# Kernel optimization log

Hardware: AMD Instinct MI355X
Metric: run time of the kernel (lower is better)

## Reference

```python
import jax, jax.numpy as jnp
import numpy as np

NEG = -1e9  # mask value for non-edges (matches masked_fill(-inf) numerically-safely)
SLOPE = 0.2  # LeakyReLU negative slope in GraphAttentionLayer


def gat_layer(x, W, a_l, a_r, adj, n_heads):
    """One GraphAttentionLayer (eval mode, is_concat=True).
    e[i,j,h] = leakyrelu(a_l . g[i,h] + a_r . g[j,h])  (attn Linear split into halves)
    softmax over j masked by adj, then aggregate neighbors.
    """
    n = x.shape[0]
    g = (x @ W).reshape(n, n_heads, -1)          # [n, h, f]
    el = jnp.einsum('ihf,f->ih', g, a_l)          # score contribution of node i
    er = jnp.einsum('jhf,f->jh', g, a_r)          # score contribution of node j
    e = jax.nn.leaky_relu(el[:, None, :] + er[None, :, :], SLOPE)  # [n, n, h]
    e = jnp.where(adj[:, :, None] != 0, e, NEG)
    a = jax.nn.softmax(e, axis=1)                 # softmax over neighbors j
    out = jnp.einsum('ijh,jhf->ihf', a, g)        # weighted aggregation
    return out.reshape(n, -1)                     # concat heads


def setup_inputs() -> dict:
    key = jax.random.key(0)
    ks = jax.random.split(key, 8)
    N, IN, HID, OUT, H = 2048, 512, 256, 128, 8
    x = jax.random.normal(ks[0], (N, IN), dtype=jnp.float32)
    adj = jax.random.randint(ks[1], (N, N), 0, 2, dtype=jnp.int32)
    adj = adj.at[jnp.arange(N), jnp.arange(N)].set(1)  # self loops: no empty softmax rows
    s = 0.05
    W1 = jax.random.normal(ks[2], (IN, HID), dtype=jnp.float32) * s
    a1_l = jax.random.normal(ks[3], (HID // H,), dtype=jnp.float32) * s
    a1_r = jax.random.normal(ks[4], (HID // H,), dtype=jnp.float32) * s
    W2 = jax.random.normal(ks[5], (HID, OUT), dtype=jnp.float32) * s
    a2_l = jax.random.normal(ks[6], (OUT,), dtype=jnp.float32) * s
    a2_r = jax.random.normal(ks[7], (OUT,), dtype=jnp.float32) * s
    return {"x": x, "W1": W1, "a1_l": a1_l, "a1_r": a1_r,
            "W2": W2, "a2_l": a2_l, "a2_r": a2_r, "adj_mat": adj}


def reference(x, W1, a1_l, a1_r, W2, a2_l, a2_r, adj_mat):
    # eval mode: nn.Dropout is identity
    h = gat_layer(x, W1, a1_l, a1_r, adj_mat, n_heads=8)
    h = jax.nn.elu(h)
    out = gat_layer(h, W2, a2_l, a2_r, adj_mat, n_heads=1)
    return out
```

## Files before the change

### kernel.cpp

```cpp
#include <hip/hip_runtime.h>
#include <hip/hip_bf16.h>

#define NN 2048
typedef unsigned short u16;
typedef unsigned long long u64;
typedef __attribute__((ext_vector_type(8))) short short8;
typedef __attribute__((ext_vector_type(4))) float f32x4;

__device__ __forceinline__ unsigned bfb(float x) {
    unsigned u = __float_as_uint(x);
    return (u + 0x7FFFu + ((u >> 16) & 1u)) >> 16;
}

__global__ __launch_bounds__(256) void prep(const float* __restrict__ x,
                                            const float* __restrict__ W1,
                                            const float* __restrict__ W2,
                                            const int* __restrict__ adj,
                                            u16* __restrict__ xb, u16* __restrict__ w1t,
                                            u16* __restrict__ w2t, u64* __restrict__ ab) {
    const int b = blockIdx.x;
    if (b < 16384) {
        int t = b * 256 + threadIdx.x;
        int W = t >> 6, lane = t & 63;
        int i = W >> 5, jw = W & 31;
        int a = adj[(size_t)i * NN + jw * 64 + lane];
        u64 m = __ballot(a != 0);
        if (lane == 0) ab[(size_t)i * 32 + jw] = m;
    } else if (b < 16384 + 1024) {
        int t = (b - 16384) * 256 + threadIdx.x;
        float4 v = ((const float4*)x)[t];
        uint2 o;
        o.x = bfb(v.x) | (bfb(v.y) << 16);
        o.y = bfb(v.z) | (bfb(v.w) << 16);
        ((uint2*)xb)[t] = o;
    } else if (b < 16384 + 1024 + 512) {
        int u = (b - 17408) * 256 + threadIdx.x;
        int c = u >> 9, k = u & 511;
        w1t[u] = (u16)bfb(W1[(size_t)k * 256 + c]);
    } else {
        int u = (b - 17920) * 256 + threadIdx.x;
        int c = u >> 8, k = u & 255;
        w2t[u] = (u16)bfb(W2[(size_t)k * 128 + c]);
    }
}

__global__ __launch_bounds__(256) void gemm1(const u16* __restrict__ A,
                                             const u16* __restrict__ BT,
                                             const float* __restrict__ al,
                                             const float* __restrict__ ar,
                                             u16* __restrict__ GT,
                                             float* __restrict__ el,
                                             float* __restrict__ ert) {
    const int i0 = blockIdx.x * 16, cs = blockIdx.y;
    const int t = threadIdx.x, lane = t & 63, w = t >> 6;
    const int q = lane >> 4, n = lane & 15;
    const int ct = w & 1, kh = w >> 1;
    __shared__ float osh[2][16][16];
    __shared__ float pel[2][16], per_[2][16];

    const u16* ap = A + (size_t)(i0 + n) * 512 + kh * 256 + q * 8;
    const u16* bp = BT + (size_t)(cs * 32 + ct * 16 + n) * 512 + kh * 256 + q * 8;
    f32x4 acc = {0.f, 0.f, 0.f, 0.f};
#pragma unroll
    for (int ks = 0; ks < 8; ++ks) {
        short8 a = *(const short8*)(ap + ks * 32);
        short8 b = *(const short8*)(bp + ks * 32);
        acc = __builtin_amdgcn_mfma_f32_16x16x32_bf16(a, b, acc, 0, 0, 0);
    }
    if (kh == 1) {
#pragma unroll
        for (int r = 0; r < 4; ++r) osh[ct][q * 4 + r][n] = acc[r];
    }
    __syncthreads();
    if (kh == 0) {
#pragma unroll
        for (int r = 0; r < 4; ++r) acc[r] += osh[ct][q * 4 + r][n];
        uint2 g0;
        g0.x = bfb(acc[0]) | (bfb(acc[1]) << 16);
        g0.y = bfb(acc[2]) | (bfb(acc[3]) << 16);
        *(uint2*)&GT[(size_t)(cs * 32 + ct * 16 + n) * NN + i0 + q * 4] = g0;
        const float alv = al[ct * 16 + n], arv = ar[ct * 16 + n];
#pragma unroll
        for (int r = 0; r < 4; ++r) {
            float ve = acc[r] * alv, vr = acc[r] * arv;
#pragma unroll
            for (int off = 1; off <= 8; off <<= 1) {
                ve += __shfl_xor(ve, off);
                vr += __shfl_xor(vr, off);
            }
            if (n == 0) { pel[ct][q * 4 + r] = ve; per_[ct][q * 4 + r] = vr; }
        }
    }
    __syncthreads();
    if (t < 16) {
        el[(size_t)(i0 + t) * 8 + cs] = pel[0][t] + pel[1][t];
        ert[(size_t)cs * NN + i0 + t] = per_[0][t] + per_[1][t];
    }
}

__global__ __launch_bounds__(256) void gemm2(const u16* __restrict__ A,
                                             const u16* __restrict__ BT,
                                             const float* __restrict__ al,
                                             const float* __restrict__ ar,
                                             u16* __restrict__ GT,
                                             float* __restrict__ el,
                                             float* __restrict__ ert) {
    const int i0 = blockIdx.x * 16, cs = blockIdx.y;
    const int t = threadIdx.x, lane = t & 63, w = t >> 6;
    const int q = lane >> 4, n = lane & 15;
    const int ct = w & 1, kh = w >> 1;
    __shared__ float osh[2][16][16];
    __shared__ float pel[2][16], per_[2][16];

    const u16* ap = A + (size_t)(i0 + n) * 256 + kh * 128 + q * 8;
    const u16* bp = BT + (size_t)(cs * 32 + ct * 16 + n) * 256 + kh * 128 + q * 8;
    f32x4 acc = {0.f, 0.f, 0.f, 0.f};
#pragma unroll
    for (int ks = 0; ks < 4; ++ks) {
        short8 a = *(const short8*)(ap + ks * 32);
        short8 b = *(const short8*)(bp + ks * 32);
        acc = __builtin_amdgcn_mfma_f32_16x16x32_bf16(a, b, acc, 0, 0, 0);
    }
    if (kh == 1) {
#pragma unroll
        for (int r = 0; r < 4; ++r) osh[ct][q * 4 + r][n] = acc[r];
    }
    __syncthreads();
    if (kh == 0) {
#pragma unroll
        for (int r = 0; r < 4; ++r) acc[r] += osh[ct][q * 4 + r][n];
        uint2 g0;
        g0.x = bfb(acc[0]) | (bfb(acc[1]) << 16);
        g0.y = bfb(acc[2]) | (bfb(acc[3]) << 16);
        *(uint2*)&GT[(size_t)(cs * 32 + ct * 16 + n) * NN + i0 + q * 4] = g0;
        const float alv = al[cs * 32 + ct * 16 + n], arv = ar[cs * 32 + ct * 16 + n];
#pragma unroll
        for (int r = 0; r < 4; ++r) {
            float ve = acc[r] * alv, vr = acc[r] * arv;
#pragma unroll
            for (int off = 1; off <= 8; off <<= 1) {
                ve += __shfl_xor(ve, off);
                vr += __shfl_xor(vr, off);
            }
            if (n == 0) { pel[ct][q * 4 + r] = ve; per_[ct][q * 4 + r] = vr; }
        }
    }
    __syncthreads();
    if (t < 16) {
        atomicAdd(&el[i0 + t], pel[0][t] + pel[1][t]);
        atomicAdd(&ert[i0 + t], per_[0][t] + per_[1][t]);
    }
}

__global__ __launch_bounds__(512) void attn1(const float* __restrict__ el,
                                             const float* __restrict__ ert,
                                             const unsigned* __restrict__ ab32,
                                             const u16* __restrict__ gbt,
                                             u16* __restrict__ hbb) {
    const int rt = blockIdx.x, sec = blockIdx.y;
    const int i0 = rt * 16, h0 = sec * 2;
    const int t = threadIdx.x, lane = t & 63, w = t >> 6;
    const int q = lane >> 4, n = lane & 15;
    const int m = t >> 5, jq = t & 31;
    const int hl = w >> 2, ch = (w >> 1) & 1, kf = w & 1;

    __shared__ __align__(16) float ers[2 * 2048];
    __shared__ __align__(16) u16 pl[2][16][72];
    __shared__ unsigned absh[16][64];
    __shared__ float psum_sh[16][2];
    __shared__ float osh[2][2][16][16];
    __shared__ float wmax[2][8];
    __shared__ float mxsh[2];

    float4 v0 = *(const float4*)(ert + (size_t)h0 * NN + t * 4);
    float4 v1 = *(const float4*)(ert + (size_t)(h0 + 1) * NN + t * 4);
    *(float4*)&ers[t * 4] = v0;
    *(float4*)&ers[2048 + t * 4] = v1;
    float m0 = fmaxf(fmaxf(v0.x, v0.y), fmaxf(v0.z, v0.w));
    float m1 = fmaxf(fmaxf(v1.x, v1.y), fmaxf(v1.z, v1.w));
#pragma unroll
    for (int off = 32; off; off >>= 1) {
        m0 = fmaxf(m0, __shfl_xor(m0, off));
        m1 = fmaxf(m1, __shfl_xor(m1, off));
    }
    if (lane == 0) { wmax[0][w] = m0; wmax[1][w] = m1; }
    for (int c = t; c < 1024; c += 512)
        absh[c >> 6][c & 63] = ab32[(size_t)(i0 + (c >> 6)) * 64 + (c & 63)];
    __syncthreads();
    if (t < 2) {
        float mm = wmax[t][0];
#pragma unroll
        for (int ww = 1; ww < 8; ++ww) mm = fmaxf(mm, wmax[t][ww]);
        mxsh[t] = mm;
    }
    __syncthreads();

    float elv[2], mxv[2], ps[2];
#pragma unroll
    for (int h = 0; h < 2; ++h) {
        float e = el[(size_t)(i0 + m) * 8 + h0 + h];
        elv[h] = e;
        float mm = e + mxsh[h];
        mxv[h] = fmaxf(mm, 0.2f * mm);
        ps[h] = 0.f;
    }
    const int col = sec * 64 + hl * 32 + ch * 16 + n;
    const u16* gb = gbt + (size_t)col * NN + kf * 32 + q * 8;
    short8 bc = *(const short8*)gb;
    f32x4 acc = {0.f, 0.f, 0.f, 0.f};

    for (int tile = 0; tile < 32; ++tile) {
        const int jt = tile * 64;
        short8 bn = bc;
        if (tile < 31) bn = *(const short8*)(gb + jt + 64);
        unsigned word = absh[m][tile * 2 + (jq >> 4)];
        unsigned bits = (word >> ((2 * jq) & 31)) & 3u;
#pragma unroll
        for (int h = 0; h < 2; ++h) {
            float2 e2 = *(const float2*)&ers[h * 2048 + jt + 2 * jq];
            float s0 = elv[h] + e2.x, s1 = elv[h] + e2.y;
            s0 = fmaxf(s0, 0.2f * s0) - mxv[h];
            s1 = fmaxf(s1, 0.2f * s1) - mxv[h];
            float p0 = (bits & 1u) ? __expf(s0) : 0.f;
            float p1 = (bits & 2u) ? __expf(s1) : 0.f;
            ps[h] += p0 + p1;
            *(unsigned*)&pl[h][m][2 * jq] = bfb(p0) | (bfb(p1) << 16);
        }
        __syncthreads();
        short8 a = *(const short8*)&pl[hl][n][kf * 32 + q * 8];
        acc = __builtin_amdgcn_mfma_f32_16x16x32_bf16(a, bc, acc, 0, 0, 0);
        bc = bn;
        __syncthreads();
    }

#pragma unroll
    for (int h = 0; h < 2; ++h) {
        float v = ps[h];
#pragma unroll
        for (int off = 16; off; off >>= 1) v += __shfl_down(v, off, 32);
        if (jq == 0) psum_sh[m][h] = v;
    }
    if (kf == 1) {
#pragma unroll
        for (int r = 0; r < 4; ++r) osh[hl][ch][q * 4 + r][n] = acc[r];
    }
    __syncthreads();
    if (kf == 0) {
#pragma unroll
        for (int r = 0; r < 4; ++r) {
            int mr = q * 4 + r;
            float o = (acc[r] + osh[hl][ch][mr][n]) / psum_sh[mr][hl];
            o = o > 0.f ? o : (__expf(o) - 1.f);
            hbb[(size_t)(i0 + mr) * 256 + col] = (u16)bfb(o);
        }
    }
}

__global__ __launch_bounds__(512) void attn2(const float* __restrict__ el,
                                             const float* __restrict__ ert,
                                             const unsigned* __restrict__ ab32,
                                             const u16* __restrict__ gbt,
                                             float* __restrict__ out) {
    const int rt = blockIdx.x, sec = blockIdx.y;
    const int i0 = rt * 16;
    const int t = threadIdx.x, lane = t & 63, w = t >> 6;
    const int q = lane >> 4, n = lane & 15;
    const int m = t >> 5, jq = t & 31;
    const int ct = w >> 2, kfr = w & 3;

    __shared__ __align__(16) float ers[2048];
    __shared__ __align__(16) u16 pl[16][136];
    __shared__ unsigned absh[16][64];
    __shared__ float psum_sh[16];
    __shared__ float osh[2][3][16][16];
    __shared__ float wmax[8];
    __shared__ float mxsh;

    float4 v0 = *(const float4*)(ert + t * 4);
    *(float4*)&ers[t * 4] = v0;
    float m0 = fmaxf(fmaxf(v0.x, v0.y), fmaxf(v0.z, v0.w));
#pragma unroll
    for (int off = 32; off; off >>= 1) m0 = fmaxf(m0, __shfl_xor(m0, off));
    if (lane == 0) wmax[w] = m0;
    for (int c = t; c < 1024; c += 512)
        absh[c >> 6][c & 63] = ab32[(size_t)(i0 + (c >> 6)) * 64 + (c & 63)];
    __syncthreads();
    if (t == 0) {
        float mm = wmax[0];
#pragma unroll
        for (int ww = 1; ww < 8; ++ww) mm = fmaxf(mm, wmax[ww]);
        mxsh = mm;
    }
    __syncthreads();

    const float elv = el[i0 + m];
    float mm2 = elv + mxsh;
    const float mxv = fmaxf(mm2, 0.2f * mm2);
    float ps = 0.f;
    const int col = sec * 32 + ct * 16 + n;
    const u16* gb = gbt + (size_t)col * NN + kfr * 32 + q * 8;
    short8 bc = *(const short8*)gb;
    f32x4 acc = {0.f, 0.f, 0.f, 0.f};

    for (int tile = 0; tile < 16; ++tile) {
        const int jt = tile * 128;
        short8 bn = bc;
        if (tile < 15) bn = *(const short8*)(gb + jt + 128);
        unsigned word = absh[m][tile * 4 + (jq >> 3)];
        unsigned bits = (word >> ((jq & 7) * 4)) & 0xFu;
        float4 e4 = *(const float4*)&ers[jt + jq * 4];
        float s0 = elv + e4.x, s1 = elv + e4.y, s2 = elv + e4.z, s3 = elv + e4.w;
        s0 = fmaxf(s0, 0.2f * s0) - mxv;
        s1 = fmaxf(s1, 0.2f * s1) - mxv;
        s2 = fmaxf(s2, 0.2f * s2) - mxv;
        s3 = fmaxf(s3, 0.2f * s3) - mxv;
        float p0 = (bits & 1u) ? __expf(s0) : 0.f;
        float p1 = (bits & 2u) ? __expf(s1) : 0.f;
        float p2 = (bits & 4u) ? __expf(s2) : 0.f;
        float p3 = (bits & 8u) ? __expf(s3) : 0.f;
        ps += (p0 + p1) + (p2 + p3);
        uint2 pk;
        pk.x = bfb(p0) | (bfb(p1) << 16);
        pk.y = bfb(p2) | (bfb(p3) << 16);
        *(uint2*)&pl[m][jq * 4] = pk;
        __syncthreads();
        short8 a = *(const short8*)&pl[n][kfr * 32 + q * 8];
        acc = __builtin_amdgcn_mfma_f32_16x16x32_bf16(a, bc, acc, 0, 0, 0);
        bc = bn;
        __syncthreads();
    }

#pragma unroll
    for (int off = 16; off; off >>= 1) ps += __shfl_down(ps, off, 32);
    if (jq == 0) psum_sh[m] = ps;
    if (kfr > 0) {
#pragma unroll
        for (int r = 0; r < 4; ++r) osh[ct][kfr - 1][q * 4 + r][n] = acc[r];
    }
    __syncthreads();
    if (kfr == 0) {
#pragma unroll
        for (int r = 0; r < 4; ++r) {
            int mr = q * 4 + r;
            float o = acc[r] + osh[ct][0][mr][n] + osh[ct][1][mr][n] + osh[ct][2][mr][n];
            out[(size_t)(i0 + mr) * 128 + col] = o / psum_sh[mr];
        }
    }
}

extern "C" void kernel_launch(void* const* d_in, const int* in_sizes, int n_in,
                              void* d_out, int out_size, void* d_ws, size_t ws_size,
                              hipStream_t stream) {
    const float* x   = (const float*)d_in[0];
    const float* W1  = (const float*)d_in[1];
    const float* a1l = (const float*)d_in[2];
    const float* a1r = (const float*)d_in[3];
    const float* W2  = (const float*)d_in[4];
    const float* a2l = (const float*)d_in[5];
    const float* a2r = (const float*)d_in[6];
    const int* adj = (const int*)d_in[7];

    char* p = (char*)d_ws;
    u16* xb    = (u16*)p;            p += (size_t)NN * 512 * 2;
    u16* w1t   = (u16*)p;            p += (size_t)256 * 512 * 2;
    u16* w2t   = (u16*)p;            p += (size_t)128 * 256 * 2;
    unsigned* abits = (unsigned*)p;  p += (size_t)NN * 64 * 4;
    u16* gbt1  = (u16*)p;            p += (size_t)256 * NN * 2;
    u16* hbb   = (u16*)p;            p += (size_t)NN * 256 * 2;
    u16* gbt2  = (u16*)p;            p += (size_t)128 * NN * 2;
    float* el1 = (float*)p;          p += (size_t)NN * 8 * 4;
    float* ert1 = (float*)p;         p += (size_t)8 * NN * 4;
    float* el2 = (float*)p;          p += (size_t)NN * 4;
    float* ert2 = (float*)p;         p += (size_t)NN * 4;

    hipMemsetAsync(el2, 0, 2 * NN * sizeof(float), stream);
    prep<<<18048, 256, 0, stream>>>(x, W1, W2, adj, xb, w1t, w2t, (u64*)abits);

    gemm1<<<dim3(128, 8), 256, 0, stream>>>(xb, w1t, a1l, a1r, gbt1, el1, ert1);
    attn1<<<dim3(128, 4), 512, 0, stream>>>(el1, ert1, abits, gbt1, hbb);

    gemm2<<<dim3(128, 4), 256, 0, stream>>>(hbb, w2t, a2l, a2r, gbt2, el2, ert2);
    attn2<<<dim3(128, 4), 512, 0, stream>>>(el2, ert2, abits, gbt2, (float*)d_out);
}
```

Measured before the change: 133.1 us.

## Double-buffer attention probability tiles and widen K tiles in GAT attention kernels

Both attention kernels now double-buffer the shared-memory probability tile, so the next tile's scores are computed while the current tile's MFMAs run, leaving one barrier per tile instead of two. attn1 moves from 64-wide to 128-wide neighbor tiles, with two MFMAs per wave per tile. attn2 is regridded to 2 column sections of 64 columns with a 2-way K split, which halves the redundant softmax work across blocks. The right-side scores are cached in LDS as bf16 rather than fp32, cutting LDS footprint at the cost of a small loss of precision in the attention logits.

```diff
diff --git a/kernel.cpp b/kernel.cpp
--- a/kernel.cpp
+++ b/kernel.cpp
@@ -11,6 +11,7 @@
     unsigned u = __float_as_uint(x);
     return (u + 0x7FFFu + ((u >> 16) & 1u)) >> 16;
 }
+__device__ __forceinline__ unsigned pk2(float a, float b) { return bfb(a) | (bfb(b) << 16); }
 
 __global__ __launch_bounds__(256) void prep(const float* __restrict__ x,
                                             const float* __restrict__ W1,
@@ -30,8 +31,8 @@
         int t = (b - 16384) * 256 + threadIdx.x;
         float4 v = ((const float4*)x)[t];
         uint2 o;
-        o.x = bfb(v.x) | (bfb(v.y) << 16);
-        o.y = bfb(v.z) | (bfb(v.w) << 16);
+        o.x = pk2(v.x, v.y);
+        o.y = pk2(v.z, v.w);
         ((uint2*)xb)[t] = o;
     } else if (b < 16384 + 1024 + 512) {
         int u = (b - 17408) * 256 + threadIdx.x;
@@ -76,8 +77,8 @@
 #pragma unroll
         for (int r = 0; r < 4; ++r) acc[r] += osh[ct][q * 4 + r][n];
         uint2 g0;
-        g0.x = bfb(acc[0]) | (bfb(acc[1]) << 16);
-        g0.y = bfb(acc[2]) | (bfb(acc[3]) << 16);
+        g0.x = pk2(acc[0], acc[1]);
+        g0.y = pk2(acc[2], acc[3]);
         *(uint2*)&GT[(size_t)(cs * 32 + ct * 16 + n) * NN + i0 + q * 4] = g0;
         const float alv = al[ct * 16 + n], arv = ar[ct * 16 + n];
 #pragma unroll
@@ -130,8 +131,8 @@
 #pragma unroll
         for (int r = 0; r < 4; ++r) acc[r] += osh[ct][q * 4 + r][n];
         uint2 g0;
-        g0.x = bfb(acc[0]) | (bfb(acc[1]) << 16);
-        g0.y = bfb(acc[2]) | (bfb(acc[3]) << 16);
+        g0.x = pk2(acc[0], acc[1]);
+        g0.y = pk2(acc[2], acc[3]);
         *(uint2*)&GT[(size_t)(cs * 32 + ct * 16 + n) * NN + i0 + q * 4] = g0;
         const float alv = al[cs * 32 + ct * 16 + n], arv = ar[cs * 32 + ct * 16 + n];
 #pragma unroll
@@ -162,10 +163,10 @@
     const int t = threadIdx.x, lane = t & 63, w = t >> 6;
     const int q = lane >> 4, n = lane & 15;
     const int m = t >> 5, jq = t & 31;
-    const int hl = w >> 2, ch = (w >> 1) & 1, kf = w & 1;
-
-    __shared__ __align__(16) float ers[2 * 2048];
-    __shared__ __align__(16) u16 pl[2][16][72];
+    const int hl = w >> 2, ch = (w >> 1) & 1, kf2 = w & 1;
+
+    __shared__ u16 ersb[2][2048];
+    __shared__ __align__(16) u16 pl[2][2][16][136];
     __shared__ unsigned absh[16][64];
     __shared__ float psum_sh[16][2];
     __shared__ float osh[2][2][16][16];
@@ -174,8 +175,11 @@
 
     float4 v0 = *(const float4*)(ert + (size_t)h0 * NN + t * 4);
     float4 v1 = *(const float4*)(ert + (size_t)(h0 + 1) * NN + t * 4);
-    *(float4*)&ers[t * 4] = v0;
-    *(float4*)&ers[2048 + t * 4] = v1;
+    uint2 c0, c1;
+    c0.x = pk2(v0.x, v0.y); c0.y = pk2(v0.z, v0.w);
+    c1.x = pk2(v1.x, v1.y); c1.y = pk2(v1.z, v1.w);
+    *(uint2*)&ersb[0][t * 4] = c0;
+    *(uint2*)&ersb[1][t * 4] = c1;
     float m0 = fmaxf(fmaxf(v0.x, v0.y), fmaxf(v0.z, v0.w));
     float m1 = fmaxf(fmaxf(v1.x, v1.y), fmaxf(v1.z, v1.w));
 #pragma unroll
@@ -204,32 +208,59 @@
         mxv[h] = fmaxf(mm, 0.2f * mm);
         ps[h] = 0.f;
     }
-    const int col = sec * 64 + hl * 32 + ch * 16 + n;
-    const u16* gb = gbt + (size_t)col * NN + kf * 32 + q * 8;
-    short8 bc = *(const short8*)gb;
-    f32x4 acc = {0.f, 0.f, 0.f, 0.f};
-
-    for (int tile = 0; tile < 32; ++tile) {
-        const int jt = tile * 64;
-        short8 bn = bc;
-        if (tile < 31) bn = *(const short8*)(gb + jt + 64);
-        unsigned word = absh[m][tile * 2 + (jq >> 4)];
-        unsigned bits = (word >> ((2 * jq) & 31)) & 3u;
+
+    auto stage = [&](int tl, int nb) {
+        unsigned word = absh[m][tl * 4 + (jq >> 3)];
+        unsigned bits = (word >> ((jq & 7) * 4)) & 0xFu;
+        const int jo = tl * 128 + jq * 4;
+        uint2 raw0 = *(const uint2*)&ersb[0][jo];
+        uint2 raw1 = *(const uint2*)&ersb[1][jo];
 #pragma unroll
         for (int h = 0; h < 2; ++h) {
-            float2 e2 = *(const float2*)&ers[h * 2048 + jt + 2 * jq];
-            float s0 = elv[h] + e2.x, s1 = elv[h] + e2.y;
+            uint2 raw = h ? raw1 : raw0;
+            float e0 = __uint_as_float(raw.x << 16);
+            float e1 = __uint_as_float(raw.x & 0xFFFF0000u);
+            float e2 = __uint_as_float(raw.y << 16);
+            float e3 = __uint_as_float(raw.y & 0xFFFF0000u);
+            float s0 = elv[h] + e0, s1 = elv[h] + e1, s2 = elv[h] + e2, s3 = elv[h] + e3;
             s0 = fmaxf(s0, 0.2f * s0) - mxv[h];
             s1 = fmaxf(s1, 0.2f * s1) - mxv[h];
+            s2 = fmaxf(s2, 0.2f * s2) - mxv[h];
+            s3 = fmaxf(s3, 0.2f * s3) - mxv[h];
             float p0 = (bits & 1u) ? __expf(s0) : 0.f;
             float p1 = (bits & 2u) ? __expf(s1) : 0.f;
-            ps[h] += p0 + p1;
-            *(unsigned*)&pl[h][m][2 * jq] = bfb(p0) | (bfb(p1) << 16);
-        }
-        __syncthreads();
-        short8 a = *(const short8*)&pl[hl][n][kf * 32 + q * 8];
-        acc = __builtin_amdgcn_mfma_f32_16x16x32_bf16(a, bc, acc, 0, 0, 0);
-        bc = bn;
+            float p2 = (bits & 4u) ? __expf(s2) : 0.f;
+            float p3 = (bits & 8u) ? __expf(s3) : 0.f;
+            ps[h] += (p0 + p1) + (p2 + p3);
+            uint2 pkv;
+            pkv.x = pk2(p0, p1);
+            pkv.y = pk2(p2, p3);
+            *(uint2*)&pl[nb][h][m][jq * 4] = pkv;
+        }
+    };
+
+    const int col = sec * 64 + hl * 32 + ch * 16 + n;
+    const u16* gb = gbt + (size_t)col * NN + kf2 * 64 + q * 8;
+    short8 bc0 = *(const short8*)gb;
+    short8 bc1 = *(const short8*)(gb + 32);
+    f32x4 acc = {0.f, 0.f, 0.f, 0.f};
+
+    stage(0, 0);
+    __syncthreads();
+
+    for (int tile = 0; tile < 16; ++tile) {
+        short8 bn0 = bc0, bn1 = bc1;
+        if (tile < 15) {
+            bn0 = *(const short8*)(gb + tile * 128 + 128);
+            bn1 = *(const short8*)(gb + tile * 128 + 160);
+        }
+        const u16* ap = &pl[tile & 1][hl][n][kf2 * 64 + q * 8];
+        short8 a0 = *(const short8*)ap;
+        short8 a1 = *(const short8*)(ap + 32);
+        acc = __builtin_amdgcn_mfma_f32_16x16x32_bf16(a0, bc0, acc, 0, 0, 0);
+        acc = __builtin_amdgcn_mfma_f32_16x16x32_bf16(a1, bc1, acc, 0, 0, 0);
+        if (tile < 15) stage(tile + 1, (tile + 1) & 1);
+        bc0 = bn0; bc1 = bn1;
         __syncthreads();
     }
 
@@ -240,12 +271,12 @@
         for (int off = 16; off; off >>= 1) v += __shfl_down(v, off, 32);
         if (jq == 0) psum_sh[m][h] = v;
     }
-    if (kf == 1) {
+    if (kf2 == 1) {
 #pragma unroll
         for (int r = 0; r < 4; ++r) osh[hl][ch][q * 4 + r][n] = acc[r];
     }
     __syncthreads();
-    if (kf == 0) {
+    if (kf2 == 0) {
 #pragma unroll
         for (int r = 0; r < 4; ++r) {
             int mr = q * 4 + r;
@@ -266,18 +297,20 @@
     const int t = threadIdx.x, lane = t & 63, w = t >> 6;
     const int q = lane >> 4, n = lane & 15;
     const int m = t >> 5, jq = t & 31;
-    const int ct = w >> 2, kfr = w & 3;
-
-    __shared__ __align__(16) float ers[2048];
-    __shared__ __align__(16) u16 pl[16][136];
+    const int ct = w >> 1, kf2 = w & 1;
+
+    __shared__ u16 ersb[2048];
+    __shared__ __align__(16) u16 pl[2][16][136];
     __shared__ unsigned absh[16][64];
     __shared__ float psum_sh[16];
-    __shared__ float osh[2][3][16][16];
+    __shared__ float osh[4][16][16];
     __shared__ float wmax[8];
     __shared__ float mxsh;
 
     float4 v0 = *(const float4*)(ert + t * 4);
-    *(float4*)&ers[t * 4] = v0;
+    uint2 c0;
+    c0.x = pk2(v0.x, v0.y); c0.y = pk2(v0.z, v0.w);
+    *(uint2*)&ersb[t * 4] = c0;
     float m0 = fmaxf(fmaxf(v0.x, v0.y), fmaxf(v0.z, v0.w));
 #pragma unroll
     for (int off = 32; off; off >>= 1) m0 = fmaxf(m0, __shfl_xor(m0, off));
@@ -297,19 +330,17 @@
     float mm2 = elv + mxsh;
     const float mxv = fmaxf(mm2, 0.2f * mm2);
     float ps = 0.f;
-    const int col = sec * 32 + ct * 16 + n;
-    const u16* gb = gbt + (size_t)col * NN + kfr * 32 + q * 8;
-    short8 bc = *(const short8*)gb;
-    f32x4 acc = {0.f, 0.f, 0.f, 0.f};
-
-    for (int tile = 0; tile < 16; ++tile) {
-        const int jt = tile * 128;
-        short8 bn = bc;
-        if (tile < 15) bn = *(const short8*)(gb + jt + 128);
-        unsigned word = absh[m][tile * 4 + (jq >> 3)];
+
+    auto stage = [&](int tl, int nb) {
+        unsigned word = absh[m][tl * 4 + (jq >> 3)];
         unsigned bits = (word >> ((jq & 7) * 4)) & 0xFu;
-        float4 e4 = *(const float4*)&ers[jt + jq * 4];
-        float s0 = elv + e4.x, s1 = elv + e4.y, s2 = elv + e4.z, s3 = elv + e4.w;
+        const int jo = tl * 128 + jq * 4;
+        uint2 raw = *(const uint2*)&ersb[jo];
+        float e0 = __uint_as_float(raw.x << 16);
+        float e1 = __uint_as_float(raw.x & 0xFFFF0000u);
+        float e2 = __uint_as_float(raw.y << 16);
+        float e3 = __uint_as_float(raw.y & 0xFFFF0000u);
+        float s0 = elv + e0, s1 = elv + e1, s2 = elv + e2, s3 = elv + e3;
         s0 = fmaxf(s0, 0.2f * s0) - mxv;
         s1 = fmaxf(s1, 0.2f * s1) - mxv;
         s2 = fmaxf(s2, 0.2f * s2) - mxv;
@@ -319,31 +350,50 @@
         float p2 = (bits & 4u) ? __expf(s2) : 0.f;
         float p3 = (bits & 8u) ? __expf(s3) : 0.f;
         ps += (p0 + p1) + (p2 + p3);
-        uint2 pk;
-        pk.x = bfb(p0) | (bfb(p1) << 16);
-        pk.y = bfb(p2) | (bfb(p3) << 16);
-        *(uint2*)&pl[m][jq * 4] = pk;
-        __syncthreads();
-        short8 a = *(const short8*)&pl[n][kfr * 32 + q * 8];
-        acc = __builtin_amdgcn_mfma_f32_16x16x32_bf16(a, bc, acc, 0, 0, 0);
-        bc = bn;
+        uint2 pkv;
+        pkv.x = pk2(p0, p1);
+        pkv.y = pk2(p2, p3);
+        *(uint2*)&pl[nb][m][jq * 4] = pkv;
+    };
+
+    const int col = sec * 64 + ct * 16 + n;
+    const u16* gb = gbt + (size_t)col * NN + kf2 * 64 + q * 8;
+    short8 bc0 = *(const short8*)gb;
+    short8 bc1 = *(const short8*)(gb + 32);
+    f32x4 acc = {0.f, 0.f, 0.f, 0.f};
+
+    stage(0, 0);
+    __syncthreads();
+
+    for (int tile = 0; tile < 16; ++tile) {
+        short8 bn0 = bc0, bn1 = bc1;
+        if (tile < 15) {
+            bn0 = *(const short8*)(gb + tile * 128 + 128);
+            bn1 = *(const short8*)(gb + tile * 128 + 160);
+        }
+        const u16* ap = &pl[tile & 1][n][kf2 * 64 + q * 8];
+        short8 a0 = *(const short8*)ap;
+        short8 a1 = *(const short8*)(ap + 32);
+        acc = __builtin_amdgcn_mfma_f32_16x16x32_bf16(a0, bc0, acc, 0, 0, 0);
+        acc = __builtin_amdgcn_mfma_f32_16x16x32_bf16(a1, bc1, acc, 0, 0, 0);
+        if (tile < 15) stage(tile + 1, (tile + 1) & 1);
+        bc0 = bn0; bc1 = bn1;
         __syncthreads();
     }
 
 #pragma unroll
     for (int off = 16; off; off >>= 1) ps += __shfl_down(ps, off, 32);
     if (jq == 0) psum_sh[m] = ps;
-    if (kfr > 0) {
-#pragma unroll
-        for (int r = 0; r < 4; ++r) osh[ct][kfr - 1][q * 4 + r][n] = acc[r];
-    }
-    __syncthreads();
-    if (kfr == 0) {
+    if (kf2 == 1) {
+#pragma unroll
+        for (int r = 0; r < 4; ++r) osh[ct][q * 4 + r][n] = acc[r];
+    }
+    __syncthreads();
+    if (kf2 == 0) {
 #pragma unroll
         for (int r = 0; r < 4; ++r) {
             int mr = q * 4 + r;
-            float o = acc[r] + osh[ct][0][mr][n] + osh[ct][1][mr][n] + osh[ct][2][mr][n];
-            out[(size_t)(i0 + mr) * 128 + col] = o / psum_sh[mr];
+            out[(size_t)(i0 + mr) * 128 + col] = (acc[r] + osh[ct][mr][n]) / psum_sh[mr];
         }
     }
 }
@@ -380,5 +430,5 @@
     attn1<<<dim3(128, 4), 512, 0, stream>>>(el1, ert1, abits, gbt1, hbb);
 
     gemm2<<<dim3(128, 4), 256, 0, stream>>>(hbb, w2t, a2l, a2r, gbt2, el2, ert2);
-    attn2<<<dim3(128, 4), 512, 0, stream>>>(el2, ert2, abits, gbt2, (float*)d_out);
-}
+    attn2<<<dim3(128, 2), 512, 0, stream>>>(el2, ert2, abits, gbt2, (float*)d_out);
+}
```

New measurement: 130.6 us. Within noise of the previous version (-1.9%).

## Split attention K-range across waves, drop per-tile LDS round-trip and barriers

Applied to the files above, without the earlier changes.

Both attention kernels now give each wave its own 256-neighbor slice of the j dimension. Each wave computes its softmax probabilities directly in registers in the MFMA A-operand layout, packs them to bf16 with a perm, and feeds them straight to the MFMA. This removes the per-tile shared-memory staging and the two __syncthreads per tile. Partial accumulators and row sums are reduced across the 8 waves through shared memory at the end. er values are stored as bf16 in LDS, the grid for attn2 is halved with 64 columns per block, and the launch bounds now request 2 blocks per CU. The costs are lower precision in er, a larger final reduction, and more LDS use.

```diff
diff --git a/kernel.cpp b/kernel.cpp
--- a/kernel.cpp
+++ b/kernel.cpp
@@ -6,11 +6,13 @@
 typedef unsigned long long u64;
 typedef __attribute__((ext_vector_type(8))) short short8;
 typedef __attribute__((ext_vector_type(4))) float f32x4;
+typedef __attribute__((ext_vector_type(4))) unsigned u32x4;
 
 __device__ __forceinline__ unsigned bfb(float x) {
     unsigned u = __float_as_uint(x);
     return (u + 0x7FFFu + ((u >> 16) & 1u)) >> 16;
 }
+__device__ __forceinline__ unsigned pk2(float a, float b) { return bfb(a) | (bfb(b) << 16); }
 
 __global__ __launch_bounds__(256) void prep(const float* __restrict__ x,
                                             const float* __restrict__ W1,
@@ -30,8 +32,8 @@
         int t = (b - 16384) * 256 + threadIdx.x;
         float4 v = ((const float4*)x)[t];
         uint2 o;
-        o.x = bfb(v.x) | (bfb(v.y) << 16);
-        o.y = bfb(v.z) | (bfb(v.w) << 16);
+        o.x = pk2(v.x, v.y);
+        o.y = pk2(v.z, v.w);
         ((uint2*)xb)[t] = o;
     } else if (b < 16384 + 1024 + 512) {
         int u = (b - 17408) * 256 + threadIdx.x;
@@ -76,8 +78,8 @@
 #pragma unroll
         for (int r = 0; r < 4; ++r) acc[r] += osh[ct][q * 4 + r][n];
         uint2 g0;
-        g0.x = bfb(acc[0]) | (bfb(acc[1]) << 16);
-        g0.y = bfb(acc[2]) | (bfb(acc[3]) << 16);
+        g0.x = pk2(acc[0], acc[1]);
+        g0.y = pk2(acc[2], acc[3]);
         *(uint2*)&GT[(size_t)(cs * 32 + ct * 16 + n) * NN + i0 + q * 4] = g0;
         const float alv = al[ct * 16 + n], arv = ar[ct * 16 + n];
 #pragma unroll
@@ -130,8 +132,8 @@
 #pragma unroll
         for (int r = 0; r < 4; ++r) acc[r] += osh[ct][q * 4 + r][n];
         uint2 g0;
-        g0.x = bfb(acc[0]) | (bfb(acc[1]) << 16);
-        g0.y = bfb(acc[2]) | (bfb(acc[3]) << 16);
+        g0.x = pk2(acc[0], acc[1]);
+        g0.y = pk2(acc[2], acc[3]);
         *(uint2*)&GT[(size_t)(cs * 32 + ct * 16 + n) * NN + i0 + q * 4] = g0;
         const float alv = al[cs * 32 + ct * 16 + n], arv = ar[cs * 32 + ct * 16 + n];
 #pragma unroll
@@ -152,30 +154,30 @@
     }
 }
 
-__global__ __launch_bounds__(512) void attn1(const float* __restrict__ el,
-                                             const float* __restrict__ ert,
-                                             const unsigned* __restrict__ ab32,
-                                             const u16* __restrict__ gbt,
-                                             u16* __restrict__ hbb) {
+__global__ __launch_bounds__(512, 2) void attn1(const float* __restrict__ el,
+                                                const float* __restrict__ ert,
+                                                const unsigned* __restrict__ ab32,
+                                                const u16* __restrict__ gbt,
+                                                u16* __restrict__ hbb) {
     const int rt = blockIdx.x, sec = blockIdx.y;
-    const int i0 = rt * 16, h0 = sec * 2;
+    const int i0 = rt * 16, h0 = sec * 2, col0 = sec * 64;
     const int t = threadIdx.x, lane = t & 63, w = t >> 6;
     const int q = lane >> 4, n = lane & 15;
-    const int m = t >> 5, jq = t & 31;
-    const int hl = w >> 2, ch = (w >> 1) & 1, kf = w & 1;
-
-    __shared__ __align__(16) float ers[2 * 2048];
-    __shared__ __align__(16) u16 pl[2][16][72];
-    __shared__ unsigned absh[16][64];
-    __shared__ float psum_sh[16][2];
-    __shared__ float osh[2][2][16][16];
+
+    __shared__ u16 ersb[2][2048];
+    __shared__ unsigned absh[16][65];
+    __shared__ float osh[8][4][16][17];
+    __shared__ float pssh[8][16][2];
     __shared__ float wmax[2][8];
     __shared__ float mxsh[2];
 
     float4 v0 = *(const float4*)(ert + (size_t)h0 * NN + t * 4);
     float4 v1 = *(const float4*)(ert + (size_t)(h0 + 1) * NN + t * 4);
-    *(float4*)&ers[t * 4] = v0;
-    *(float4*)&ers[2048 + t * 4] = v1;
+    uint2 c0, c1;
+    c0.x = pk2(v0.x, v0.y); c0.y = pk2(v0.z, v0.w);
+    c1.x = pk2(v1.x, v1.y); c1.y = pk2(v1.z, v1.w);
+    *(uint2*)&ersb[0][t * 4] = c0;
+    *(uint2*)&ersb[1][t * 4] = c1;
     float m0 = fmaxf(fmaxf(v0.x, v0.y), fmaxf(v0.z, v0.w));
     float m1 = fmaxf(fmaxf(v1.x, v1.y), fmaxf(v1.z, v1.w));
 #pragma unroll
@@ -198,86 +200,103 @@
     float elv[2], mxv[2], ps[2];
 #pragma unroll
     for (int h = 0; h < 2; ++h) {
-        float e = el[(size_t)(i0 + m) * 8 + h0 + h];
+        float e = el[(size_t)(i0 + n) * 8 + h0 + h];
         elv[h] = e;
         float mm = e + mxsh[h];
         mxv[h] = fmaxf(mm, 0.2f * mm);
         ps[h] = 0.f;
     }
-    const int col = sec * 64 + hl * 32 + ch * 16 + n;
-    const u16* gb = gbt + (size_t)col * NN + kf * 32 + q * 8;
-    short8 bc = *(const short8*)gb;
-    f32x4 acc = {0.f, 0.f, 0.f, 0.f};
-
-    for (int tile = 0; tile < 32; ++tile) {
-        const int jt = tile * 64;
-        short8 bn = bc;
-        if (tile < 31) bn = *(const short8*)(gb + jt + 64);
-        unsigned word = absh[m][tile * 2 + (jq >> 4)];
-        unsigned bits = (word >> ((2 * jq) & 31)) & 3u;
+    f32x4 acc[4];
+#pragma unroll
+    for (int ct = 0; ct < 4; ++ct) acc[ct] = (f32x4){0.f, 0.f, 0.f, 0.f};
+
+    const int kb = w * 256;
+    const u16* gbp = gbt + (size_t)(col0 + n) * NN + kb + q * 8;
+
+#pragma unroll
+    for (int ck = 0; ck < 8; ++ck) {
+        const int jb = ck * 32;
+        unsigned word = absh[n][(kb + jb) >> 5];
+        unsigned bits = (word >> (q * 8)) & 0xFFu;
+        short8 bv0 = *(const short8*)(gbp + jb);
+        short8 bv1 = *(const short8*)(gbp + 16 * NN + jb);
+        short8 bv2 = *(const short8*)(gbp + 32 * NN + jb);
+        short8 bv3 = *(const short8*)(gbp + 48 * NN + jb);
+        short8 af[2];
 #pragma unroll
         for (int h = 0; h < 2; ++h) {
-            float2 e2 = *(const float2*)&ers[h * 2048 + jt + 2 * jq];
-            float s0 = elv[h] + e2.x, s1 = elv[h] + e2.y;
-            s0 = fmaxf(s0, 0.2f * s0) - mxv[h];
-            s1 = fmaxf(s1, 0.2f * s1) - mxv[h];
-            float p0 = (bits & 1u) ? __expf(s0) : 0.f;
-            float p1 = (bits & 2u) ? __expf(s1) : 0.f;
-            ps[h] += p0 + p1;
-            *(unsigned*)&pl[h][m][2 * jq] = bfb(p0) | (bfb(p1) << 16);
+            u32x4 raw = *(const u32x4*)&ersb[h][kb + jb + q * 8];
+            u32x4 au;
+#pragma unroll
+            for (int pr = 0; pr < 4; ++pr) {
+                unsigned u = raw[pr];
+                float e0 = __uint_as_float(u << 16);
+                float e1 = __uint_as_float(u & 0xFFFF0000u);
+                float s0 = elv[h] + e0, s1 = elv[h] + e1;
+                s0 = fmaxf(s0, 0.2f * s0) - mxv[h];
+                s1 = fmaxf(s1, 0.2f * s1) - mxv[h];
+                float p0 = __expf(s0), p1 = __expf(s1);
+                p0 = ((bits >> (2 * pr)) & 1u) ? p0 : 0.f;
+                p1 = ((bits >> (2 * pr + 1)) & 1u) ? p1 : 0.f;
+                unsigned b0 = __float_as_uint(p0) & 0xFFFF0000u;
+                unsigned b1 = __float_as_uint(p1) & 0xFFFF0000u;
+                ps[h] += __uint_as_float(b0) + __uint_as_float(b1);
+                au[pr] = __builtin_amdgcn_perm(__float_as_uint(p1), __float_as_uint(p0), 0x07060302u);
+            }
+            af[h] = __builtin_bit_cast(short8, au);
         }
-        __syncthreads();
-        short8 a = *(const short8*)&pl[hl][n][kf * 32 + q * 8];
-        acc = __builtin_amdgcn_mfma_f32_16x16x32_bf16(a, bc, acc, 0, 0, 0);
-        bc = bn;
-        __syncthreads();
+        acc[0] = __builtin_amdgcn_mfma_f32_16x16x32_bf16(af[0], bv0, acc[0], 0, 0, 0);
+        acc[1] = __builtin_amdgcn_mfma_f32_16x16x32_bf16(af[0], bv1, acc[1], 0, 0, 0);
+        acc[2] = __builtin_amdgcn_mfma_f32_16x16x32_bf16(af[1], bv2, acc[2], 0, 0, 0);
+        acc[3] = __builtin_amdgcn_mfma_f32_16x16x32_bf16(af[1], bv3, acc[3], 0, 0, 0);
     }
 
 #pragma unroll
     for (int h = 0; h < 2; ++h) {
         float v = ps[h];
-#pragma unroll
-        for (int off = 16; off; off >>= 1) v += __shfl_down(v, off, 32);
-        if (jq == 0) psum_sh[m][h] = v;
-    }
-    if (kf == 1) {
-#pragma unroll
-        for (int r = 0; r < 4; ++r) osh[hl][ch][q * 4 + r][n] = acc[r];
-    }
-    __syncthreads();
-    if (kf == 0) {
-#pragma unroll
-        for (int r = 0; r < 4; ++r) {
-            int mr = q * 4 + r;
-            float o = (acc[r] + osh[hl][ch][mr][n]) / psum_sh[mr][hl];
-            o = o > 0.f ? o : (__expf(o) - 1.f);
-            hbb[(size_t)(i0 + mr) * 256 + col] = (u16)bfb(o);
-        }
-    }
-}
-
-__global__ __launch_bounds__(512) void attn2(const float* __restrict__ el,
-                                             const float* __restrict__ ert,
-                                             const unsigned* __restrict__ ab32,
-                                             const u16* __restrict__ gbt,
-                                             float* __restrict__ out) {
+        v += __shfl_xor(v, 16);
+        v += __shfl_xor(v, 32);
+        if (q == 0) pssh[w][n][h] = v;
+    }
+#pragma unroll
+    for (int ct = 0; ct < 4; ++ct)
+#pragma unroll
+        for (int r = 0; r < 4; ++r) osh[w][ct][q * 4 + r][n] = acc[ct][r];
+    __syncthreads();
+
+    for (int idx = t; idx < 1024; idx += 512) {
+        int ct = idx >> 8, mm = (idx >> 4) & 15, nn = idx & 15;
+        int hh = ct >> 1;
+        float o = 0.f, pv = 0.f;
+#pragma unroll
+        for (int ww = 0; ww < 8; ++ww) { o += osh[ww][ct][mm][nn]; pv += pssh[ww][mm][hh]; }
+        o /= pv;
+        o = o > 0.f ? o : (__expf(o) - 1.f);
+        hbb[(size_t)(i0 + mm) * 256 + col0 + ct * 16 + nn] = (u16)bfb(o);
+    }
+}
+
+__global__ __launch_bounds__(512, 2) void attn2(const float* __restrict__ el,
+                                                const float* __restrict__ ert,
+                                                const unsigned* __restrict__ ab32,
+                                                const u16* __restrict__ gbt,
+                                                float* __restrict__ out) {
     const int rt = blockIdx.x, sec = blockIdx.y;
-    const int i0 = rt * 16;
+    const int i0 = rt * 16, col0 = sec * 64;
     const int t = threadIdx.x, lane = t & 63, w = t >> 6;
     const int q = lane >> 4, n = lane & 15;
-    const int m = t >> 5, jq = t & 31;
-    const int ct = w >> 2, kfr = w & 3;
-
-    __shared__ __align__(16) float ers[2048];
-    __shared__ __align__(16) u16 pl[16][136];
-    __shared__ unsigned absh[16][64];
-    __shared__ float psum_sh[16];
-    __shared__ float osh[2][3][16][16];
+
+    __shared__ u16 ersb[2048];
+    __shared__ unsigned absh[16][65];
+    __shared__ float osh[8][4][16][17];
+    __shared__ float pssh[8][16];
     __shared__ float wmax[8];
     __shared__ float mxsh;
 
     float4 v0 = *(const float4*)(ert + t * 4);
-    *(float4*)&ers[t * 4] = v0;
+    uint2 c0;
+    c0.x = pk2(v0.x, v0.y); c0.y = pk2(v0.z, v0.w);
+    *(uint2*)&ersb[t * 4] = c0;
     float m0 = fmaxf(fmaxf(v0.x, v0.y), fmaxf(v0.z, v0.w));
 #pragma unroll
     for (int off = 32; off; off >>= 1) m0 = fmaxf(m0, __shfl_xor(m0, off));
@@ -293,58 +312,69 @@
     }
     __syncthreads();
 
-    const float elv = el[i0 + m];
+    const float elv = el[i0 + n];
     float mm2 = elv + mxsh;
     const float mxv = fmaxf(mm2, 0.2f * mm2);
     float ps = 0.f;
-    const int col = sec * 32 + ct * 16 + n;
-    const u16* gb = gbt + (size_t)col * NN + kfr * 32 + q * 8;
-    short8 bc = *(const short8*)gb;
-    f32x4 acc = {0.f, 0.f, 0.f, 0.f};
-
-    for (int tile = 0; tile < 16; ++tile) {
-        const int jt = tile * 128;
-        short8 bn = bc;
-        if (tile < 15) bn = *(const short8*)(gb + jt + 128);
-        unsigned word = absh[m][tile * 4 + (jq >> 3)];
-        unsigned bits = (word >> ((jq & 7) * 4)) & 0xFu;
-        float4 e4 = *(const float4*)&ers[jt + jq * 4];
-        float s0 = elv + e4.x, s1 = elv + e4.y, s2 = elv + e4.z, s3 = elv + e4.w;
-        s0 = fmaxf(s0, 0.2f * s0) - mxv;
-        s1 = fmaxf(s1, 0.2f * s1) - mxv;
-        s2 = fmaxf(s2, 0.2f * s2) - mxv;
-        s3 = fmaxf(s3, 0.2f * s3) - mxv;
-        float p0 = (bits & 1u) ? __expf(s0) : 0.f;
-        float p1 = (bits & 2u) ? __expf(s1) : 0.f;
-        float p2 = (bits & 4u) ? __expf(s2) : 0.f;
-        float p3 = (bits & 8u) ? __expf(s3) : 0.f;
-        ps += (p0 + p1) + (p2 + p3);
-        uint2 pk;
-        pk.x = bfb(p0) | (bfb(p1) << 16);
-        pk.y = bfb(p2) | (bfb(p3) << 16);
-        *(uint2*)&pl[m][jq * 4] = pk;
-        __syncthreads();
-        short8 a = *(const short8*)&pl[n][kfr * 32 + q * 8];
-        acc = __builtin_amdgcn_mfma_f32_16x16x32_bf16(a, bc, acc, 0, 0, 0);
-        bc = bn;
-        __syncthreads();
-    }
-
-#pragma unroll
-    for (int off = 16; off; off >>= 1) ps += __shfl_down(ps, off, 32);
-    if (jq == 0) psum_sh[m] = ps;
-    if (kfr > 0) {
-#pragma unroll
-        for (int r = 0; r < 4; ++r) osh[ct][kfr - 1][q * 4 + r][n] = acc[r];
-    }
-    __syncthreads();
-    if (kfr == 0) {
-#pragma unroll
-        for (int r = 0; r < 4; ++r) {
-            int mr = q * 4 + r;
-            float o = acc[r] + osh[ct][0][mr][n] + osh[ct][1][mr][n] + osh[ct][2][mr][n];
-            out[(size_t)(i0 + mr) * 128 + col] = o / psum_sh[mr];
+    f32x4 acc[4];
+#pragma unroll
+    for (int ct = 0; ct < 4; ++ct) acc[ct] = (f32x4){0.f, 0.f, 0.f, 0.f};
+
+    const int kb = w * 256;
+    const u16* gbp = gbt + (size_t)(col0 + n) * NN + kb + q * 8;
+
+#pragma unroll
+    for (int ck = 0; ck < 8; ++ck) {
+        const int jb = ck * 32;
+        unsigned word = absh[n][(kb + jb) >> 5];
+        unsigned bits = (word >> (q * 8)) & 0xFFu;
+        short8 bv0 = *(const short8*)(gbp + jb);
+        short8 bv1 = *(const short8*)(gbp + 16 * NN + jb);
+        short8 bv2 = *(const short8*)(gbp + 32 * NN + jb);
+        short8 bv3 = *(const short8*)(gbp + 48 * NN + jb);
+        u32x4 raw = *(const u32x4*)&ersb[kb + jb + q * 8];
+        u32x4 au;
+#pragma unroll
+        for (int pr = 0; pr < 4; ++pr) {
+            unsigned u = raw[pr];
+            float e0 = __uint_as_float(u << 16);
+            float e1 = __uint_as_float(u & 0xFFFF0000u);
+            float s0 = elv + e0, s1 = elv + e1;
+            s0 = fmaxf(s0, 0.2f * s0) - mxv;
+            s1 = fmaxf(s1, 0.2f * s1) - mxv;
+            float p0 = __expf(s0), p1 = __expf(s1);
+            p0 = ((bits >> (2 * pr)) & 1u) ? p0 : 0.f;
+            p1 = ((bits >> (2 * pr + 1)) & 1u) ? p1 : 0.f;
+            unsigned b0 = __float_as_uint(p0) & 0xFFFF0000u;
+            unsigned b1 = __float_as_uint(p1) & 0xFFFF0000u;
+            ps += __uint_as_float(b0) + __uint_as_float(b1);
+            au[pr] = __builtin_amdgcn_perm(__float_as_uint(p1), __float_as_uint(p0), 0x07060302u);
         }
+        short8 af = __builtin_bit_cast(short8, au);
+        acc[0] = __builtin_amdgcn_mfma_f32_16x16x32_bf16(af, bv0, acc[0], 0, 0, 0);
+        acc[1] = __builtin_amdgcn_mfma_f32_16x16x32_bf16(af, bv1, acc[1], 0, 0, 0);
+        acc[2] = __builtin_amdgcn_mfma_f32_16x16x32_bf16(af, bv2, acc[2], 0, 0, 0);
+        acc[3] = __builtin_amdgcn_mfma_f32_16x16x32_bf16(af, bv3, acc[3], 0, 0, 0);
+    }
+
+    {
+        float v = ps;
+        v += __shfl_xor(v, 16);
+        v += __shfl_xor(v, 32);
+        if (q == 0) pssh[w][n] = v;
+    }
+#pragma unroll
+    for (int ct = 0; ct < 4; ++ct)
+#pragma unroll
+        for (int r = 0; r < 4; ++r) osh[w][ct][q * 4 + r][n] = acc[ct][r];
+    __syncthreads();
+
+    for (int idx = t; idx < 1024; idx += 512) {
+        int ct = idx >> 8, mm = (idx >> 4) & 15, nn = idx & 15;
+        float o = 0.f, pv = 0.f;
+#pragma unroll
+        for (int ww = 0; ww < 8; ++ww) { o += osh[ww][ct][mm][nn]; pv += pssh[ww][mm]; }
+        out[(size_t)(i0 + mm) * 128 + col0 + ct * 16 + nn] = o / pv;
     }
 }
 
@@ -380,5 +410,5 @@
     attn1<<<dim3(128, 4), 512, 0, stream>>>(el1, ert1, abits, gbt1, hbb);
 
     gemm2<<<dim3(128, 4), 256, 0, stream>>>(hbb, w2t, a2l, a2r, gbt2, el2, ert2);
-    attn2<<<dim3(128, 4), 512, 0, stream>>>(el2, ert2, abits, gbt2, (float*)d_out);
-}
+    attn2<<<dim3(128, 2), 512, 0, stream>>>(el2, ert2, abits, gbt2, (float*)d_out);
+}
```

After: 132.6 us. No clear change (-0.4%).
